# Performance work log

Measured on AMD Instinct MI355X. Metric: run time of the kernel, lower is better.

## Reference

```python
import jax, jax.numpy as jnp
import numpy as np

BN_EPS = 1e-5


def _bn(h, gamma, beta):
    # torch BatchNorm1d training-mode forward: biased batch variance
    mu = h.mean(axis=0)
    var = h.var(axis=0)
    return (h - mu) * jax.lax.rsqrt(var + BN_EPS) * gamma + beta


def setup_inputs() -> dict:
    N, E, H = 100000, 1600000, 128
    HID = 2 * H  # get_torch_mlp hidden_channels = 2*out_channels = 256
    key = jax.random.key(0)
    ks = jax.random.split(key, 8)
    s_lin = 1.0 / np.sqrt(H)
    s_mlp = 1.0 / np.sqrt(2 * H)
    return {
        "x": jax.random.normal(ks[0], (N, H), dtype=jnp.float32),
        "edge_index": jax.random.randint(ks[1], (2, E), 0, N, dtype=jnp.int64),
        "lin_w": jax.random.normal(ks[2], (2 * H, H), dtype=jnp.float32) * s_lin,
        "lin_b": jnp.zeros((2 * H,), dtype=jnp.float32),
        "eps": jnp.zeros((), dtype=jnp.float32),
        "w1": jax.random.normal(ks[3], (HID, 2 * H), dtype=jnp.float32) * s_mlp,
        "g1": jnp.ones((HID,), dtype=jnp.float32),
        "b1": jnp.zeros((HID,), dtype=jnp.float32),
        "w2": jax.random.normal(ks[4], (HID, HID), dtype=jnp.float32) * (1.0 / np.sqrt(HID)),
        "g2": jnp.ones((HID,), dtype=jnp.float32),
        "b2": jnp.zeros((HID,), dtype=jnp.float32),
        "w3": jax.random.normal(ks[5], (H, HID), dtype=jnp.float32) * (1.0 / np.sqrt(HID)),
        "b3": jnp.zeros((H,), dtype=jnp.float32),
    }


def reference(x, edge_index, lin_w, lin_b, eps, w1, g1, b1, w2, g2, b2, w3, b3):
    N = x.shape[0]
    dst, src = edge_index[0], edge_index[1]
    # transfer1(atoms, G): irregular gather of neighbor rows + scatter-add,
    # duplicated across the two order-1 linmap channel blocks -> [N, 2H]
    agg = jax.ops.segment_sum(x[src], dst, num_segments=N)
    x_transfer = jnp.concatenate([agg, agg], axis=-1)
    # linmaps1 on singleton domains: [broadcast(sum)=x, id=x] -> [N, 2H]
    x_linmaps = jnp.concatenate([x, x], axis=-1)
    x_lin = x @ lin_w.T + lin_b
    h = x_lin + (1.0 + eps) * x_linmaps + x_transfer  # stack([...]).sum(0)
    # MLP: Linear(no bias) -> BN -> ReLU -> Linear(no bias) -> BN -> ReLU -> Linear(bias)
    h = jax.nn.relu(_bn(h @ w1.T, g1, b1))
    h = jax.nn.relu(_bn(h @ w2.T, g2, b2))
    h = h @ w3.T + b3
    return h  # rows of the output ptensors1 (same atoms)
```

## Files before the change

### kernel.cpp

```cpp
#include <hip/hip_runtime.h>
#include <cstdint>
#include <cstddef>

typedef __bf16 bf16_t;
typedef __bf16 bf16x8 __attribute__((ext_vector_type(8)));
typedef float f32x4 __attribute__((ext_vector_type(4)));

#define GLOBAL_AS __attribute__((address_space(1)))
#define LDS_AS    __attribute__((address_space(3)))

__device__ __forceinline__ void glds16(const void* g, void* l) {
    __builtin_amdgcn_global_load_lds((const GLOBAL_AS void*)g, (LDS_AS void*)l, 16, 0, 0);
}

__device__ __forceinline__ float bf2f(unsigned short u) {
    union { unsigned int i; float f; } c; c.i = ((unsigned int)u) << 16; return c.f;
}

__global__ void conv_k(const float* __restrict__ in, bf16_t* __restrict__ out, int n8) {
    int id = blockIdx.x * 256 + threadIdx.x;
    if (id >= n8) return;
    const float4* p = (const float4*)in;
    float4 a = p[2 * id], b = p[2 * id + 1];
    bf16x8 o;
    o[0] = (bf16_t)a.x; o[1] = (bf16_t)a.y; o[2] = (bf16_t)a.z; o[3] = (bf16_t)a.w;
    o[4] = (bf16_t)b.x; o[5] = (bf16_t)b.y; o[6] = (bf16_t)b.z; o[7] = (bf16_t)b.w;
    *(bf16x8*)(out + (size_t)id * 8) = o;
}

__global__ void conv_x_k(const float* __restrict__ in, bf16_t* __restrict__ ha, int n8) {
    int id = blockIdx.x * 256 + threadIdx.x;
    if (id >= n8) return;
    const float4* p = (const float4*)in;
    float4 a = p[2 * id], b = p[2 * id + 1];
    bf16x8 o;
    o[0] = (bf16_t)a.x; o[1] = (bf16_t)a.y; o[2] = (bf16_t)a.z; o[3] = (bf16_t)a.w;
    o[4] = (bf16_t)b.x; o[5] = (bf16_t)b.y; o[6] = (bf16_t)b.z; o[7] = (bf16_t)b.w;
    int row = id >> 4, ch = id & 15;
    *(bf16x8*)(ha + (size_t)row * 256 + ch * 8) = o;
}

__global__ void wcomb_k(const float* __restrict__ w1, const float* __restrict__ lin_w,
                        const float* __restrict__ lin_b, const float* __restrict__ eps_p,
                        bf16_t* __restrict__ wc, float* __restrict__ bcomb) {
    __shared__ float red[256];
    int c = blockIdx.x, t = threadIdx.x;
    const float* w1row = w1 + c * 256;
    float onepe = 1.f + *eps_p;
    float v;
    if (t < 128) {
        float acc = 0.f;
        for (int j = 0; j < 256; j++) acc += w1row[j] * lin_w[j * 128 + t];
        v = acc + onepe * (w1row[t] + w1row[t + 128]);
    } else {
        int m = t - 128;
        v = w1row[m] + w1row[t];
    }
    wc[c * 256 + t] = (bf16_t)v;
    red[t] = w1row[t] * lin_b[t];
    __syncthreads();
    for (int off = 128; off > 0; off >>= 1) {
        if (t < off) red[t] += red[t + off];
        __syncthreads();
    }
    if (t == 0) bcomb[c] = red[0];
}

__global__ void detect_k(const int* __restrict__ ei, int* __restrict__ flag) {
    int v = ei[2 * threadIdx.x + 1];
    if (v != 0) atomicOr(flag, 1);
}

#define CHUNK 8192

__global__ __launch_bounds__(256) void bhist_k(const void* __restrict__ ei, const int* __restrict__ flag,
                                               int E, int* __restrict__ bcnt) {
    __shared__ int cnt[1024];
    int t = threadIdx.x;
    for (int b = t; b < 1024; b += 256) cnt[b] = 0;
    __syncthreads();
    int base = blockIdx.x * CHUNK;
    int i32 = *flag;
#pragma unroll 4
    for (int i = 0; i < CHUNK / 256; i++) {
        int e = base + t + 256 * i;
        if (e < E) {
            int dst = i32 ? ((const int*)ei)[e] : (int)((const long long*)ei)[e];
            atomicAdd(&cnt[dst >> 7], 1);
        }
    }
    __syncthreads();
    for (int b = t; b < 1024; b += 256)
        if (cnt[b]) atomicAdd(&bcnt[b], cnt[b]);
}

__global__ __launch_bounds__(1024) void bscan_k(const int* __restrict__ bcnt, int* __restrict__ boffs,
                                                int* __restrict__ gcur, int* __restrict__ offs,
                                                int NBK, int N, int E) {
    __shared__ int lds[1024];
    int t = threadIdx.x;
    int v = (t < NBK) ? bcnt[t] : 0;
    lds[t] = v;
    __syncthreads();
    for (int off = 1; off < 1024; off <<= 1) {
        int add = (t >= off) ? lds[t - off] : 0;
        __syncthreads();
        lds[t] += add;
        __syncthreads();
    }
    if (t < NBK) {
        int excl = lds[t] - v;
        boffs[t] = excl;
        gcur[t] = excl;
    }
    if (t == 0) { boffs[NBK] = E; offs[N] = E; }
}

__global__ __launch_bounds__(256) void binfill_k(const void* __restrict__ ei, const int* __restrict__ flag,
                                                 int E, int NBK, int* __restrict__ gcur,
                                                 unsigned* __restrict__ pairs) {
    __shared__ int cnt[1024];
    __shared__ int pref[1024];
    __shared__ int cur[1024];
    __shared__ int gbase[1024];
    __shared__ int red[256];
    __shared__ unsigned slot[CHUNK];
    __shared__ unsigned short sbk[CHUNK];
    int t = threadIdx.x;
    int base = blockIdx.x * CHUNK;
    int chunk_n = E - base; if (chunk_n > CHUNK) chunk_n = CHUNK;
    int i32 = *flag;
    for (int b = t; b < 1024; b += 256) cnt[b] = 0;
    __syncthreads();
#pragma unroll 4
    for (int i = 0; i < CHUNK / 256; i++) {
        int e = base + t + 256 * i;
        if (e < E) {
            int dst = i32 ? ((const int*)ei)[e] : (int)((const long long*)ei)[e];
            atomicAdd(&cnt[dst >> 7], 1);
        }
    }
    __syncthreads();
    int t4 = t * 4;
    int c0 = cnt[t4], c1 = cnt[t4 + 1], c2 = cnt[t4 + 2], c3 = cnt[t4 + 3];
    int s = c0 + c1 + c2 + c3;
    red[t] = s;
    __syncthreads();
    for (int off = 1; off < 256; off <<= 1) {
        int add = (t >= off) ? red[t - off] : 0;
        __syncthreads();
        red[t] += add;
        __syncthreads();
    }
    int run = red[t] - s;
    pref[t4] = run; cur[t4] = run; run += c0;
    pref[t4 + 1] = run; cur[t4 + 1] = run; run += c1;
    pref[t4 + 2] = run; cur[t4 + 2] = run; run += c2;
    pref[t4 + 3] = run; cur[t4 + 3] = run;
    __syncthreads();
#pragma unroll 4
    for (int i = 0; i < CHUNK / 256; i++) {
        int e = base + t + 256 * i;
        if (e < E) {
            int dst, src;
            if (i32) { dst = ((const int*)ei)[e]; src = ((const int*)ei)[E + e]; }
            else     { dst = (int)((const long long*)ei)[e]; src = (int)((const long long*)ei)[E + e]; }
            int b = dst >> 7;
            int p = atomicAdd(&cur[b], 1);
            slot[p] = ((unsigned)(dst & 127) << 20) | (unsigned)src;
            sbk[p] = (unsigned short)b;
        }
    }
    __syncthreads();
    for (int b = t; b < 1024; b += 256) {
        int c = (b + 1 < 1024) ? (pref[b + 1] - pref[b]) : (chunk_n - pref[b]);
        if (b < NBK && c > 0) gbase[b] = atomicAdd(&gcur[b], c);
    }
    __syncthreads();
    for (int i = t; i < chunk_n; i += 256) {
        int bk = sbk[i];
        pairs[gbase[bk] + (i - pref[bk])] = slot[i];
    }
}

__global__ __launch_bounds__(256) void bsort2_k(const unsigned* __restrict__ pairs,
                                                const int* __restrict__ boffs,
                                                int* __restrict__ offs,
                                                int* __restrict__ csr, int N) {
    __shared__ int cnt[128], pref[128], cur[128];
    int t = threadIdx.x;
    int b = blockIdx.x;
    int s = boffs[b], e = boffs[b + 1];
    if (t < 128) cnt[t] = 0;
    __syncthreads();
    for (int i = s + t; i < e; i += 256)
        atomicAdd(&cnt[pairs[i] >> 20], 1);
    __syncthreads();
    if (t < 128) pref[t] = cnt[t];
    __syncthreads();
    for (int off = 1; off < 128; off <<= 1) {
        int v = 0;
        if (t < 128 && t >= off) v = pref[t - off];
        __syncthreads();
        if (t < 128) pref[t] += v;
        __syncthreads();
    }
    if (t < 128) {
        int ex = pref[t] - cnt[t];
        cur[t] = ex;
        int node = b * 128 + t;
        if (node < N) offs[node] = s + ex;
    }
    __syncthreads();
    for (int i = s + t; i < e; i += 256) {
        unsigned u = pairs[i];
        int dl = (int)(u >> 20);
        int p = atomicAdd(&cur[dl], 1);
        csr[s + p] = (int)((u & 0xFFFFFu) << 9);
    }
}

__global__ __launch_bounds__(256) void gather_k(bf16_t* __restrict__ ha, const int* __restrict__ offs,
                                                const int* __restrict__ csr, int N) {
    int w = (blockIdx.x * 256 + threadIdx.x) >> 6;
    if (w >= N) return;
    int lane = threadIdx.x & 63;
    int g = lane >> 4, l15 = lane & 15;
    int s = offs[w], e = offs[w + 1];
    float acc[8] = {0.f, 0.f, 0.f, 0.f, 0.f, 0.f, 0.f, 0.f};
    float acc2[8] = {0.f, 0.f, 0.f, 0.f, 0.f, 0.f, 0.f, 0.f};
    int i = s + g;
    bool h0 = i < e, h1 = i + 4 < e;
    int p0 = h0 ? csr[i] : 0;
    int p1 = h1 ? csr[i + 4] : 0;
    while (h1) {
        int ni = i + 8;
        bool nh0 = ni < e, nh1 = ni + 4 < e;
        int np0 = nh0 ? csr[ni] : 0;
        int np1 = nh1 ? csr[ni + 4] : 0;
        bf16x8 v0 = *(const bf16x8*)((const char*)ha + (size_t)(unsigned)p0 + l15 * 16);
        bf16x8 v1 = *(const bf16x8*)((const char*)ha + (size_t)(unsigned)p1 + l15 * 16);
#pragma unroll
        for (int j = 0; j < 8; j++) { acc[j] += (float)v0[j]; acc2[j] += (float)v1[j]; }
        i = ni; p0 = np0; p1 = np1; h0 = nh0; h1 = nh1;
    }
    if (h0) {
        bf16x8 v0 = *(const bf16x8*)((const char*)ha + (size_t)(unsigned)p0 + l15 * 16);
#pragma unroll
        for (int j = 0; j < 8; j++) acc[j] += (float)v0[j];
    }
#pragma unroll
    for (int j = 0; j < 8; j++) {
        acc[j] += acc2[j];
        acc[j] += __shfl_xor(acc[j], 16);
        acc[j] += __shfl_xor(acc[j], 32);
    }
    if (g == 0) {
        bf16x8 o;
#pragma unroll
        for (int j = 0; j < 8; j++) o[j] = (bf16_t)acc[j];
        *(bf16x8*)(ha + (size_t)w * 256 + 128 + l15 * 8) = o;
    }
}

template<int NCOLTOT, bool BNIN, bool STATS, bool FINAL, bool BIAS>
__global__ __launch_bounds__(512, 4) void gemm_q(
    const bf16_t* __restrict__ A, const bf16_t* __restrict__ W,
    const unsigned* __restrict__ scshp,
    float* __restrict__ sums, float* __restrict__ sqs,
    const float* __restrict__ bias,
    bf16_t* __restrict__ Obf, float* __restrict__ Of, int N, int ntiles, int shift)
{
    __shared__ __align__(16) char smemW[32768];
    __shared__ __align__(16) char smemA[32768];

    const int tid = threadIdx.x;
    const int lane = tid & 63, wid = tid >> 6;
    const int l15 = lane & 15, l4 = lane >> 4;
    const int rowg = wid & 1, colg = wid >> 1;
    const int tstride = 1 << shift;
    const int colq = (int)blockIdx.x >> shift;
    const int rb = (int)blockIdx.x & (tstride - 1);

#pragma unroll
    for (int it = 0; it < 4; it++) {
        int d = (it * 512 + tid) * 16;
        int col = d >> 9, koff = d & 511;
        int ksw = koff ^ ((col & 7) << 4);
        glds16((const char*)W + (size_t)(colq * 64 + col) * 512 + ksw, smemW + d);
    }

    unsigned sslp[32];
    if constexpr (BNIN) {
#pragma unroll
        for (int it = 0; it < 4; it++) {
            int d = (it * 512 + tid) * 16;
            int k0 = (d & 511) >> 1;
#pragma unroll
            for (int i = 0; i < 8; i++) sslp[it * 8 + i] = scshp[k0 + i];
        }
    }

    bf16x8 rA[4];
    auto loadA = [&](int t) {
        size_t rowbase = (size_t)t * 64;
#pragma unroll
        for (int it = 0; it < 4; it++) {
            int d = (it * 512 + tid) * 16;
            int row = d >> 9, koff = d & 511;
            rA[it] = *(const bf16x8*)((const char*)A + (rowbase + row) * 512 + koff);
        }
    };
    auto transformR = [&]() {
#pragma unroll
        for (int it = 0; it < 4; it++) {
            bf16x8 v = rA[it], o;
#pragma unroll
            for (int i = 0; i < 8; i++) {
                unsigned p = sslp[it * 8 + i];
                float sc = bf2f((unsigned short)(p & 0xffff));
                float sh = bf2f((unsigned short)(p >> 16));
                o[i] = (bf16_t)fmaxf((float)v[i] * sc + sh, 0.f);
            }
            rA[it] = o;
        }
    };
    auto writeA = [&]() {
#pragma unroll
        for (int it = 0; it < 4; it++) {
            int d = (it * 512 + tid) * 16;
            int row = d >> 9, koff = d & 511;
            *(bf16x8*)(smemA + row * 512 + (koff ^ ((row & 7) << 4))) = rA[it];
        }
    };

    const int colw = colq * 64 + colg * 16 + l15;
    float bbv = 0.f;
    if constexpr (BIAS || FINAL) bbv = bias[colw];
    float sA = 0.f, qA = 0.f;

    f32x4 acc[2];

    auto compute = [&]() {
        acc[0] = f32x4{0.f, 0.f, 0.f, 0.f};
        acc[1] = f32x4{0.f, 0.f, 0.f, 0.f};
        const int col = colg * 16 + l15;
        const int wsw = (col & 7) << 4;
#pragma unroll
        for (int c = 0; c < 8; c++) {
            const int koff = c * 64 + l4 * 16;
            bf16x8 a0, a1;
            {
                int row = rowg * 32 + l15;
                a0 = *(const bf16x8*)(smemA + row * 512 + (koff ^ ((row & 7) << 4)));
                row += 16;
                a1 = *(const bf16x8*)(smemA + row * 512 + (koff ^ ((row & 7) << 4)));
            }
            const bf16x8 b = *(const bf16x8*)(smemW + col * 512 + (koff ^ wsw));
            acc[0] = __builtin_amdgcn_mfma_f32_16x16x32_bf16(a0, b, acc[0], 0, 0, 0);
            acc[1] = __builtin_amdgcn_mfma_f32_16x16x32_bf16(a1, b, acc[1], 0, 0, 0);
        }
    };

    auto epilogue = [&](int t) {
        const int rows0 = t * 64 + rowg * 32;
#pragma unroll
        for (int fr = 0; fr < 2; fr++) {
            int rb0 = rows0 + fr * 16 + l4 * 4;
            f32x4 av = acc[fr];
#pragma unroll
            for (int i = 0; i < 4; i++) {
                int r = rb0 + i;
                if constexpr (FINAL) {
                    if (r < N) Of[(size_t)r * NCOLTOT + colw] = av[i] + bbv;
                } else {
                    float v = av[i];
                    if constexpr (BIAS) v += bbv;
                    bf16_t hv = (bf16_t)v;
                    if (r < N) Obf[(size_t)r * 256 + colw] = hv;
                    if constexpr (STATS) {
                        float vv = (r < N) ? (float)hv : 0.f;
                        sA += vv; qA += vv * vv;
                    }
                }
            }
        }
    };

    int t = rb;
    if (t < ntiles) {
        loadA(t);
        if constexpr (BNIN) transformR();
        writeA();
    }
    __syncthreads();

    while (t < ntiles) {
        int tn = t + tstride;
        if (tn < ntiles) loadA(tn);
        compute();
        epilogue(t);
        __syncthreads();
        if (tn < ntiles) {
            if constexpr (BNIN) transformR();
            writeA();
        }
        __syncthreads();
        t = tn;
    }

    if constexpr (STATS) {
        sA += __shfl_xor(sA, 16); sA += __shfl_xor(sA, 32);
        qA += __shfl_xor(qA, 16); qA += __shfl_xor(qA, 32);
        if (lane < 16) {
            atomicAdd(&sums[colw], sA);
            atomicAdd(&sqs[colw], qA);
        }
    }
}

__global__ void finalize_k(const float* __restrict__ sum, const float* __restrict__ sq,
                           const float* __restrict__ g, const float* __restrict__ b,
                           unsigned* __restrict__ scshp, float invN) {
    int t = threadIdx.x;
    float mean = sum[t] * invN;
    float var = sq[t] * invN - mean * mean;
    float s = g[t] * rsqrtf(var + 1e-5f);
    float sh = b[t] - mean * s;
    unsigned short us = __builtin_bit_cast(unsigned short, (bf16_t)s);
    unsigned short uh = __builtin_bit_cast(unsigned short, (bf16_t)sh);
    scshp[t] = (unsigned)us | ((unsigned)uh << 16);
}

extern "C" void kernel_launch(void* const* d_in, const int* in_sizes, int n_in,
                              void* d_out, int out_size, void* d_ws, size_t ws_size,
                              hipStream_t stream)
{
    const int N = in_sizes[0] / 128;
    const int E = in_sizes[1] / 2;
    const float* x     = (const float*)d_in[0];
    const void*  ei    = d_in[1];
    const float* lin_w = (const float*)d_in[2];
    const float* lin_b = (const float*)d_in[3];
    const float* eps   = (const float*)d_in[4];
    const float* w1    = (const float*)d_in[5];
    const float* g1    = (const float*)d_in[6];
    const float* b1    = (const float*)d_in[7];
    const float* w2    = (const float*)d_in[8];
    const float* g2    = (const float*)d_in[9];
    const float* b2    = (const float*)d_in[10];
    const float* w3    = (const float*)d_in[11];
    const float* b3    = (const float*)d_in[12];
    float* out = (float*)d_out;

    char* ws = (char*)d_ws;
    size_t o = 0;
    auto alloc = [&](size_t bytes) -> char* {
        char* p = ws + o;
        o = (o + bytes + 255) & ~(size_t)255;
        return p;
    };
    bf16_t*   ha    = (bf16_t*)alloc((size_t)N * 256 * 2);
    bf16_t*   hb    = (bf16_t*)alloc((size_t)N * 256 * 2);
    bf16_t*   wcb   = (bf16_t*)alloc((size_t)256 * 256 * 2);
    bf16_t*   w2b   = (bf16_t*)alloc((size_t)256 * 256 * 2);
    bf16_t*   w3b   = (bf16_t*)alloc((size_t)128 * 256 * 2);
    float*    bcomb = (float*)alloc(256 * 4);
    float*    stats = (float*)alloc(4 * 256 * 4);
    unsigned* scshp1 = (unsigned*)alloc(256 * 4);
    unsigned* scshp2 = (unsigned*)alloc(256 * 4);
    int*      bcnt  = (int*)alloc(1024 * 4);
    int*      boffs = (int*)alloc(1025 * 4);
    int*      gcur  = (int*)alloc(1024 * 4);
    int*      offs  = (int*)alloc((size_t)(N + 1) * 4);
    unsigned* pairs = (unsigned*)alloc((size_t)E * 4);
    int*      csr   = (int*)alloc((size_t)E * 4);
    int*      flag  = (int*)alloc(4);

    const int NBK = (N + 127) >> 7;

    hipMemsetAsync(bcnt, 0, 1024 * 4, stream);
    hipMemsetAsync(stats, 0, 4 * 256 * 4, stream);
    hipMemsetAsync(flag, 0, 4, stream);

    int nx8 = N * 16;
    conv_x_k<<<(nx8 + 255) / 256, 256, 0, stream>>>(x, ha, nx8);
    wcomb_k<<<256, 256, 0, stream>>>(w1, lin_w, lin_b, eps, wcb, bcomb);
    conv_k<<<32, 256, 0, stream>>>(w2, w2b, 8192);
    conv_k<<<16, 256, 0, stream>>>(w3, w3b, 4096);

    const int nch = (E + CHUNK - 1) / CHUNK;
    detect_k<<<1, 256, 0, stream>>>((const int*)ei, flag);
    bhist_k<<<nch, 256, 0, stream>>>(ei, flag, E, bcnt);
    bscan_k<<<1, 1024, 0, stream>>>(bcnt, boffs, gcur, offs, NBK, N, E);
    binfill_k<<<nch, 256, 0, stream>>>(ei, flag, E, NBK, gcur, pairs);
    bsort2_k<<<NBK, 256, 0, stream>>>(pairs, boffs, offs, csr, N);
    gather_k<<<(N + 3) / 4, 256, 0, stream>>>(ha, offs, csr, N);

    const int nt64 = (N + 63) / 64;
    gemm_q<256, false, true, false, true><<<512, 512, 0, stream>>>(
        ha, wcb, nullptr, stats + 0, stats + 256, bcomb, hb, nullptr, N, nt64, 7);
    finalize_k<<<1, 256, 0, stream>>>(stats + 0, stats + 256, g1, b1, scshp1, 1.f / (float)N);
    gemm_q<256, true, true, false, false><<<512, 512, 0, stream>>>(
        hb, w2b, scshp1, stats + 512, stats + 768, nullptr, ha, nullptr, N, nt64, 7);
    finalize_k<<<1, 256, 0, stream>>>(stats + 512, stats + 768, g2, b2, scshp2, 1.f / (float)N);
    gemm_q<128, true, false, true, true><<<512, 512, 0, stream>>>(
        ha, w3b, scshp2, nullptr, nullptr, b3, nullptr, out, N, nt64, 8);
}
```

Measured before the change: 251.5 us.

## Keep W fragments in registers and double-buffer A tiles via async LDS loads

Each wave now holds its slice of the weight matrix as register-resident MFMA B fragments instead of staging W in shared memory. The freed LDS becomes a double buffer for A, filled with direct global-to-LDS loads that overlap with compute on the other buffer. The BN+ReLU input transform is now done in place in LDS, with scale/shift indices adjusted for the swizzle. This drops the register round trip and one barrier per tile in the non-BN path, at the cost of more VGPRs per thread and an extra LDS read/write pass in the BN path.

```diff
diff --git a/kernel.cpp b/kernel.cpp
--- a/kernel.cpp
+++ b/kernel.cpp
@@ -271,8 +271,7 @@
     const float* __restrict__ bias,
     bf16_t* __restrict__ Obf, float* __restrict__ Of, int N, int ntiles, int shift)
 {
-    __shared__ __align__(16) char smemW[32768];
-    __shared__ __align__(16) char smemA[32768];
+    __shared__ __align__(16) char smemA[2][32768];
 
     const int tid = threadIdx.x;
     const int lane = tid & 63, wid = tid >> 6;
@@ -282,39 +281,42 @@
     const int colq = (int)blockIdx.x >> shift;
     const int rb = (int)blockIdx.x & (tstride - 1);
 
-#pragma unroll
-    for (int it = 0; it < 4; it++) {
-        int d = (it * 512 + tid) * 16;
-        int col = d >> 9, koff = d & 511;
-        int ksw = koff ^ ((col & 7) << 4);
-        glds16((const char*)W + (size_t)(colq * 64 + col) * 512 + ksw, smemW + d);
-    }
-
-    unsigned sslp[32];
-    if constexpr (BNIN) {
-#pragma unroll
-        for (int it = 0; it < 4; it++) {
-            int d = (it * 512 + tid) * 16;
-            int k0 = (d & 511) >> 1;
-#pragma unroll
-            for (int i = 0; i < 8; i++) sslp[it * 8 + i] = scshp[k0 + i];
-        }
-    }
-
-    bf16x8 rA[4];
-    auto loadA = [&](int t) {
+    const int colw = colq * 64 + colg * 16 + l15;
+
+    bf16x8 bfrag[8];
+#pragma unroll
+    for (int c = 0; c < 8; c++)
+        bfrag[c] = *(const bf16x8*)(W + (size_t)colw * 256 + c * 32 + l4 * 8);
+
+    auto stageA = [&](int buf, int t) {
         size_t rowbase = (size_t)t * 64;
 #pragma unroll
         for (int it = 0; it < 4; it++) {
             int d = (it * 512 + tid) * 16;
             int row = d >> 9, koff = d & 511;
-            rA[it] = *(const bf16x8*)((const char*)A + (rowbase + row) * 512 + koff);
+            int ksw = koff ^ ((row & 7) << 4);
+            glds16((const char*)A + (rowbase + row) * 512 + ksw, smemA[buf] + d);
         }
     };
-    auto transformR = [&]() {
+
+    unsigned sslp[32];
+    if constexpr (BNIN) {
 #pragma unroll
         for (int it = 0; it < 4; it++) {
-            bf16x8 v = rA[it], o;
+            int d = (it * 512 + tid) * 16;
+            int row = d >> 9;
+            int k0 = ((d & 511) ^ ((row & 7) << 4)) >> 1;
+#pragma unroll
+            for (int i = 0; i < 8; i++) sslp[it * 8 + i] = scshp[k0 + i];
+        }
+    }
+
+    auto transformA = [&](int buf) {
+#pragma unroll
+        for (int it = 0; it < 4; it++) {
+            int d = (it * 512 + tid) * 16;
+            bf16x8 v = *(const bf16x8*)(smemA[buf] + d);
+            bf16x8 o;
 #pragma unroll
             for (int i = 0; i < 8; i++) {
                 unsigned p = sslp[it * 8 + i];
@@ -322,43 +324,31 @@
                 float sh = bf2f((unsigned short)(p >> 16));
                 o[i] = (bf16_t)fmaxf((float)v[i] * sc + sh, 0.f);
             }
-            rA[it] = o;
+            *(bf16x8*)(smemA[buf] + d) = o;
         }
     };
-    auto writeA = [&]() {
-#pragma unroll
-        for (int it = 0; it < 4; it++) {
-            int d = (it * 512 + tid) * 16;
-            int row = d >> 9, koff = d & 511;
-            *(bf16x8*)(smemA + row * 512 + (koff ^ ((row & 7) << 4))) = rA[it];
-        }
-    };
-
-    const int colw = colq * 64 + colg * 16 + l15;
+
     float bbv = 0.f;
     if constexpr (BIAS || FINAL) bbv = bias[colw];
     float sA = 0.f, qA = 0.f;
 
     f32x4 acc[2];
 
-    auto compute = [&]() {
+    auto compute = [&](int buf) {
         acc[0] = f32x4{0.f, 0.f, 0.f, 0.f};
         acc[1] = f32x4{0.f, 0.f, 0.f, 0.f};
-        const int col = colg * 16 + l15;
-        const int wsw = (col & 7) << 4;
 #pragma unroll
         for (int c = 0; c < 8; c++) {
             const int koff = c * 64 + l4 * 16;
             bf16x8 a0, a1;
             {
                 int row = rowg * 32 + l15;
-                a0 = *(const bf16x8*)(smemA + row * 512 + (koff ^ ((row & 7) << 4)));
+                a0 = *(const bf16x8*)(smemA[buf] + row * 512 + (koff ^ ((row & 7) << 4)));
                 row += 16;
-                a1 = *(const bf16x8*)(smemA + row * 512 + (koff ^ ((row & 7) << 4)));
+                a1 = *(const bf16x8*)(smemA[buf] + row * 512 + (koff ^ ((row & 7) << 4)));
             }
-            const bf16x8 b = *(const bf16x8*)(smemW + col * 512 + (koff ^ wsw));
-            acc[0] = __builtin_amdgcn_mfma_f32_16x16x32_bf16(a0, b, acc[0], 0, 0, 0);
-            acc[1] = __builtin_amdgcn_mfma_f32_16x16x32_bf16(a1, b, acc[1], 0, 0, 0);
+            acc[0] = __builtin_amdgcn_mfma_f32_16x16x32_bf16(a0, bfrag[c], acc[0], 0, 0, 0);
+            acc[1] = __builtin_amdgcn_mfma_f32_16x16x32_bf16(a1, bfrag[c], acc[1], 0, 0, 0);
         }
     };
 
@@ -387,25 +377,25 @@
         }
     };
 
-    int t = rb;
-    if (t < ntiles) {
-        loadA(t);
-        if constexpr (BNIN) transformR();
-        writeA();
-    }
-    __syncthreads();
+    int t = rb, buf = 0;
+    if (t < ntiles) stageA(0, t);
+    __syncthreads();
+    if constexpr (BNIN) {
+        if (t < ntiles) transformA(0);
+        __syncthreads();
+    }
 
     while (t < ntiles) {
         int tn = t + tstride;
-        if (tn < ntiles) loadA(tn);
-        compute();
+        if (tn < ntiles) stageA(buf ^ 1, tn);
+        compute(buf);
         epilogue(t);
         __syncthreads();
-        if (tn < ntiles) {
-            if constexpr (BNIN) transformR();
-            writeA();
-        }
-        __syncthreads();
+        if constexpr (BNIN) {
+            if (tn < ntiles) transformA(buf ^ 1);
+            __syncthreads();
+        }
+        buf ^= 1;
         t = tn;
     }
 
```

After: 249.7 us. No clear change (-0.7%).
